# Optimization experiments

Measured on AMD Instinct MI355X. Metric: run time of the kernel, lower is better.

The kernel has to match this reference:

```python
import jax, jax.numpy as jnp
import numpy as np

B, D, T = 2048, 512, 100  # batch_dim, state_dim, number of time points


def setup_inputs() -> dict:
    key = jax.random.key(0)
    k1, k2 = jax.random.split(key)
    y0 = 0.1 * jax.random.normal(k1, (B, D), dtype=jnp.float32)
    ts = jnp.arange(T, dtype=jnp.float32) * 0.01  # monotone time grid
    noise = jax.random.normal(k2, (T - 1, B, D), dtype=jnp.float32)  # standard-normal Brownian draws
    theta = jnp.float32(0.1)  # learned scalar parameter
    return {"y0": y0, "ts": ts, "noise": noise, "theta": theta}


def reference(y0, ts, noise, theta):
    # Euler-Maruyama integration of dy = f(t,y) dt + g(t,y) dW (diagonal noise)
    #   f(t, y) = sin(t) + theta * y
    #   g(t, y) = 0.3 * sigmoid(cos(t) * exp(-y))
    dts = ts[1:] - ts[:-1]          # [T-1]
    t_left = ts[:-1]                # [T-1] left endpoint times

    def step(y, inp):
        t, dt, z = inp
        drift = jnp.sin(t) + theta * y
        diff = 0.3 * jax.nn.sigmoid(jnp.cos(t) * jnp.exp(-y))
        y_next = y + drift * dt + diff * jnp.sqrt(dt) * z
        return y_next, y_next

    _, traj = jax.lax.scan(step, y0, (t_left, dts, noise))
    # sdeint returns the solution at every t, including t0
    return jnp.concatenate([y0[None], traj], axis=0)  # [T, B, D]
```

## Files before the change

### kernel.cpp

```cpp
#include <hip/hip_runtime.h>
#include <math.h>

#define MAX_T 128

__global__ __launch_bounds__(256) void sde_kernel(
    const float* __restrict__ y0,
    const float* __restrict__ ts,
    const float* __restrict__ noise,
    const float* __restrict__ theta_p,
    float* __restrict__ out,
    int n4, int T)
{
    __shared__ float s_sin[MAX_T], s_cos[MAX_T], s_dt[MAX_T], s_sqdt[MAX_T];
    int tid = threadIdx.x;
    if (tid < T - 1) {
        float t  = ts[tid];
        float dt = ts[tid + 1] - t;
        s_sin[tid]  = sinf(t);
        s_cos[tid]  = cosf(t);
        s_dt[tid]   = dt;
        s_sqdt[tid] = sqrtf(dt);
    }
    float theta = theta_p[0];
    __syncthreads();

    int idx = blockIdx.x * blockDim.x + threadIdx.x;
    if (idx >= n4) return;

    const float4* __restrict__ y0v  = (const float4*)y0;
    const float4* __restrict__ nv   = (const float4*)noise;
    float4* __restrict__       outv = (float4*)out;

    float4 y = y0v[idx];
    outv[idx] = y;

    float4 z = nv[idx];
    for (int t = 0; t < T - 1; ++t) {
        float4 znext = make_float4(0.f, 0.f, 0.f, 0.f);
        if (t + 1 < T - 1)
            znext = nv[(size_t)(t + 1) * n4 + idx];

        float st = s_sin[t];
        float ct = s_cos[t];
        float dt = s_dt[t];
        float sq = s_sqdt[t];

        #define STEP(c) { \
            float drift = st + theta * y.c; \
            float e   = __expf(-y.c); \
            float arg = ct * e; \
            float sig = __builtin_amdgcn_rcpf(1.0f + __expf(-arg)); \
            float diff = 0.3f * sig; \
            y.c = y.c + drift * dt + diff * sq * z.c; }
        STEP(x); STEP(y); STEP(z); STEP(w);
        #undef STEP

        outv[(size_t)(t + 1) * n4 + idx] = y;
        z = znext;
    }
}

extern "C" void kernel_launch(void* const* d_in, const int* in_sizes, int n_in,
                              void* d_out, int out_size, void* d_ws, size_t ws_size,
                              hipStream_t stream) {
    const float* y0    = (const float*)d_in[0];
    const float* ts    = (const float*)d_in[1];
    const float* noise = (const float*)d_in[2];
    const float* theta = (const float*)d_in[3];
    float* out = (float*)d_out;

    int n = in_sizes[0];
    int T = in_sizes[1];
    int n4 = n / 4;

    int block = 256;
    int grid = (n4 + block - 1) / block;
    sde_kernel<<<grid, block, 0, stream>>>(y0, ts, noise, theta, out, n4, T);
}
```

Measured before the change: 660.8 us.

## Prefetch noise four steps ahead with nontemporal loads/stores and fold step constants

Restructures the time loop into a 4-deep rotating register prefetch of noise so more loads are in flight per thread. It also uses nontemporal loads and stores for the streaming noise and output, and precomputes per-step constants (1+theta*dt, sin*dt, cos, 0.3*sqrt(dt)) into one vectorized shared-memory entry, so the update becomes two FMAs. The kernel is bandwidth-bound, so the gain depends on better latency hiding and cache bypass. The cost is higher register pressure.

```diff
diff --git a/kernel.cpp b/kernel.cpp
--- a/kernel.cpp
+++ b/kernel.cpp
@@ -2,6 +2,8 @@
 #include <math.h>
 
 #define MAX_T 128
+
+typedef float f4 __attribute__((ext_vector_type(4)));
 
 __global__ __launch_bounds__(256) void sde_kernel(
     const float* __restrict__ y0,
@@ -11,53 +13,64 @@
     float* __restrict__ out,
     int n4, int T)
 {
-    __shared__ float s_sin[MAX_T], s_cos[MAX_T], s_dt[MAX_T], s_sqdt[MAX_T];
+    __shared__ f4 s_c[MAX_T];
     int tid = threadIdx.x;
+    float theta = theta_p[0];
     if (tid < T - 1) {
         float t  = ts[tid];
         float dt = ts[tid + 1] - t;
-        s_sin[tid]  = sinf(t);
-        s_cos[tid]  = cosf(t);
-        s_dt[tid]   = dt;
-        s_sqdt[tid] = sqrtf(dt);
+        f4 c;
+        c.x = 1.0f + theta * dt;
+        c.y = sinf(t) * dt;
+        c.z = cosf(t);
+        c.w = 0.3f * sqrtf(dt);
+        s_c[tid] = c;
     }
-    float theta = theta_p[0];
     __syncthreads();
 
     int idx = blockIdx.x * blockDim.x + threadIdx.x;
     if (idx >= n4) return;
 
-    const float4* __restrict__ y0v  = (const float4*)y0;
-    const float4* __restrict__ nv   = (const float4*)noise;
-    float4* __restrict__       outv = (float4*)out;
+    const f4* __restrict__ y0v = (const f4*)y0;
+    const f4* __restrict__ nv  = (const f4*)noise;
+    f4* __restrict__       outv = (f4*)out;
 
-    float4 y = y0v[idx];
-    outv[idx] = y;
+    f4 y = y0v[idx];
+    __builtin_nontemporal_store(y, &outv[idx]);
 
-    float4 z = nv[idx];
-    for (int t = 0; t < T - 1; ++t) {
-        float4 znext = make_float4(0.f, 0.f, 0.f, 0.f);
-        if (t + 1 < T - 1)
-            znext = nv[(size_t)(t + 1) * n4 + idx];
+    const int NT = T - 1;
 
-        float st = s_sin[t];
-        float ct = s_cos[t];
-        float dt = s_dt[t];
-        float sq = s_sqdt[t];
+    f4 zinit = {0.f, 0.f, 0.f, 0.f};
+    f4 z0 = zinit, z1 = zinit, z2 = zinit, z3 = zinit;
+    if (0 < NT) z0 = __builtin_nontemporal_load(&nv[idx]);
+    if (1 < NT) z1 = __builtin_nontemporal_load(&nv[(size_t)n4 + idx]);
+    if (2 < NT) z2 = __builtin_nontemporal_load(&nv[(size_t)2 * n4 + idx]);
+    if (3 < NT) z3 = __builtin_nontemporal_load(&nv[(size_t)3 * n4 + idx]);
 
-        #define STEP(c) { \
-            float drift = st + theta * y.c; \
-            float e   = __expf(-y.c); \
-            float arg = ct * e; \
-            float sig = __builtin_amdgcn_rcpf(1.0f + __expf(-arg)); \
-            float diff = 0.3f * sig; \
-            y.c = y.c + drift * dt + diff * sq * z.c; }
-        STEP(x); STEP(y); STEP(z); STEP(w);
-        #undef STEP
+    #define ELEM(comp) { \
+        float e   = __expf(-y.comp); \
+        float sig = __builtin_amdgcn_rcpf(1.0f + __expf(-(c.z * e))); \
+        y.comp = fmaf(c.w * sig, zz.comp, fmaf(y.comp, c.x, c.y)); }
 
-        outv[(size_t)(t + 1) * n4 + idx] = y;
-        z = znext;
+    #define BODY(Z, tt) { \
+        if ((tt) < NT) { \
+            f4 c  = s_c[(tt)]; \
+            f4 zz = Z; \
+            if ((tt) + 4 < NT) \
+                Z = __builtin_nontemporal_load(&nv[(size_t)((tt) + 4) * n4 + idx]); \
+            ELEM(x); ELEM(y); ELEM(z); ELEM(w); \
+            __builtin_nontemporal_store(y, &outv[(size_t)((tt) + 1) * n4 + idx]); \
+        } }
+
+    for (int t = 0; t < NT; t += 4) {
+        BODY(z0, t);
+        BODY(z1, t + 1);
+        BODY(z2, t + 2);
+        BODY(z3, t + 3);
     }
+
+    #undef BODY
+    #undef ELEM
 }
 
 extern "C" void kernel_launch(void* const* d_in, const int* in_sizes, int n_in,
```

After: 647.1 us. 2.1% less time.
